# Optimization experiments

Hardware: AMD Instinct MI355X
Metric: run time of the kernel (lower is better)

Reference implementation:

```python
import jax, jax.numpy as jnp
import numpy as np

N = 50000        # nodes
E = 1600000      # edges (before self loops)
IN_DIM = 300     # input feature size
HID = 256        # hidden size
HEADS = 8
OC = HID // HEADS  # out channels per head = 32
LAYERS = 4
B = 1024         # number of target pairs
C = 3            # num classes
NEG_SLOPE = 0.2  # PyG GATConv leaky_relu slope


def setup_inputs() -> dict:
    key = jax.random.key(0)
    ks = jax.random.split(key, 12)

    def glorot(k, shape):
        lim = np.sqrt(6.0 / (shape[-2] + shape[-1]))
        return jax.random.uniform(k, shape, jnp.float32, -lim, lim)

    return {
        "x": jax.random.normal(ks[0], (N, IN_DIM), jnp.float32),
        "edge_index": jax.random.randint(ks[1], (2, E), 0, N, jnp.int64 if jax.config.jax_enable_x64 else jnp.int32),
        "target_mask": jax.random.randint(ks[2], (B, 2), 0, N, jnp.int64 if jax.config.jax_enable_x64 else jnp.int32),
        # lin1: [IN_DIM, HID] (stored pre-transposed vs torch)
        "lin1_W": glorot(ks[3], (IN_DIM, HID)),
        "lin1_b": jnp.zeros((HID,), jnp.float32),
        # stacked GATConv params
        "convs_W": glorot(ks[4], (LAYERS, HID, HEADS * OC)),
        "convs_att_dst": glorot(ks[5], (LAYERS, HEADS, OC)),  # att half applied to x_i (target)
        "convs_att_src": glorot(ks[6], (LAYERS, HEADS, OC)),  # att half applied to x_j (source)
        "convs_b": jnp.zeros((LAYERS, HID), jnp.float32),
        # lin3: [2*HID, C]
        "lin3_W": glorot(ks[7], (2 * HID, C)),
        "lin3_b": jnp.zeros((C,), jnp.float32),
    }


def gat_layer(h, src, tgt, W, att_dst, att_src, bias):
    """PyG-style GATConv (concat heads), edge list already includes self loops.
    h: [N, HID]; src/tgt: [E+N]; W: [HID, HEADS*OC]."""
    hw = (h @ W).reshape(N, HEADS, OC)
    # per-node attention scores, gathered per-edge (avoids materializing concat features)
    s_dst = jnp.einsum("nho,ho->nh", hw, att_dst)  # score for target role
    s_src = jnp.einsum("nho,ho->nh", hw, att_src)  # score for source role
    alpha = jax.nn.leaky_relu(s_dst[tgt] + s_src[src], NEG_SLOPE)  # [Etot, HEADS]
    # softmax over edges sharing the same target node (self loops => no empty segments)
    m = jax.ops.segment_max(alpha, tgt, num_segments=N)
    ex = jnp.exp(alpha - m[tgt])
    denom = jax.ops.segment_sum(ex, tgt, num_segments=N)
    a = ex / (denom[tgt] + 1e-16)
    # weighted scatter-aggregate of source features
    out = jax.ops.segment_sum(hw[src] * a[:, :, None], tgt, num_segments=N)  # [N, HEADS, OC]
    return out.reshape(N, HEADS * OC) + bias


def reference(x, edge_index, target_mask, lin1_W, lin1_b, convs_W,
              convs_att_dst, convs_att_src, convs_b, lin3_W, lin3_b):
    # add self loops once (PyG GATConv does this per layer; same edge set every layer)
    loop = jnp.arange(N, dtype=edge_index.dtype)
    src = jnp.concatenate([edge_index[0], loop])
    tgt = jnp.concatenate([edge_index[1], loop])

    h = x @ lin1_W + lin1_b
    for l in range(LAYERS):
        h = jax.nn.elu(gat_layer(h, src, tgt, convs_W[l],
                                 convs_att_dst[l], convs_att_src[l], convs_b[l]))
    # gather the two target nodes per sample and flatten -> [B, 2*HID]
    feats = h[target_mask].reshape(B, 2 * HID)
    logits = feats @ lin3_W + lin3_b
    return logits
```

## Files before the change

kernel.cpp:

```cpp
#include <hip/hip_runtime.h>
#include <math.h>

#define N_NODES 50000
#define N_PAD   50048
#define E_EDGES 1600000
#define ETOT    (E_EDGES + N_NODES)
#define EPAD    (E_EDGES + 8 * N_NODES)
#define IN_DIM  300
#define KP1     320
#define HID     256
#define HEADS   8
#define OC      32
#define LAYERS  4
#define BSAMP   1024
#define NEG_SLOPE 0.2f
#define DEG_CAP 128

#define NB     8
#define NPB    6250
#define BCAP   262144
#define NBLK_P 512

typedef unsigned long long ull;
typedef _Float16 half8 __attribute__((ext_vector_type(8)));
typedef _Float16 half4v __attribute__((ext_vector_type(4)));
typedef float f32x4 __attribute__((ext_vector_type(4)));


__global__ __launch_bounds__(256) void part_count_kernel(const int* __restrict__ tgt,
                                                         int* __restrict__ gcount) {
    __shared__ int cnt[NB];
    if (threadIdx.x < NB) cnt[threadIdx.x] = 0;
    __syncthreads();
    const int chunk = (ETOT + NBLK_P - 1) / NBLK_P;
    int beg = blockIdx.x * chunk;
    int end = min(beg + chunk, ETOT);
    for (int e = beg + threadIdx.x; e < end; e += 256) {
        int t_ = (e < E_EDGES) ? tgt[e] : (e - E_EDGES);
        atomicAdd(&cnt[t_ / NPB], 1);
    }
    __syncthreads();
    if (threadIdx.x < NB) gcount[blockIdx.x * NB + threadIdx.x] = cnt[threadIdx.x];
}

__global__ __launch_bounds__(64) void part_scan_kernel(const int* __restrict__ gcount,
                                                       int* __restrict__ goff,
                                                       int* __restrict__ bcnt) {
    int b = threadIdx.x;
    if (b >= NB) return;
    int running = 0;
    for (int k = 0; k < NBLK_P; k++) {
        goff[k * NB + b] = running;
        running += gcount[k * NB + b];
    }
    bcnt[b] = running;
}

__global__ __launch_bounds__(256) void part_scatter_kernel(const int* __restrict__ src,
                                                           const int* __restrict__ tgt,
                                                           const int* __restrict__ goff,
                                                           ull* __restrict__ bpart) {
    __shared__ int cur[NB];
    if (threadIdx.x < NB) cur[threadIdx.x] = goff[blockIdx.x * NB + threadIdx.x];
    __syncthreads();
    const int chunk = (ETOT + NBLK_P - 1) / NBLK_P;
    int beg = blockIdx.x * chunk;
    int end = min(beg + chunk, ETOT);
    for (int e = beg + threadIdx.x; e < end; e += 256) {
        int s_, t_;
        if (e < E_EDGES) { s_ = src[e]; t_ = tgt[e]; }
        else             { s_ = t_ = e - E_EDGES; }
        int b = t_ / NPB;
        int pos = atomicAdd(&cur[b], 1);
        bpart[(size_t)b * BCAP + pos] = ((ull)(unsigned)t_ << 32) | (unsigned)s_;
    }
}

__global__ __launch_bounds__(256) void count_edges_kernel(const ull* __restrict__ bpart,
                                                          const int* __restrict__ bcnt,
                                                          int* counts) {
    int b = blockIdx.x & (NB - 1);
    int ib = blockIdx.x >> 3;
    int nblk = gridDim.x >> 3;
    int nb = bcnt[b];
    const ull* bp = bpart + (size_t)b * BCAP;
    for (int i = ib * 256 + threadIdx.x; i < nb; i += nblk * 256)
        atomicAdd(&counts[(int)(bp[i] >> 32)], 1);
}

__global__ __launch_bounds__(256) void scan_kernel(const int* __restrict__ counts,
                                                   int* __restrict__ row_ptr,
                                                   int* __restrict__ cursor) {
    __shared__ int sums[256];
    const int CHUNK = (N_NODES + 255) / 256;
    int t = threadIdx.x;
    int beg = t * CHUNK;
    int fin = min(beg + CHUNK, N_NODES);
    int s = 0;
    for (int i = beg; i < fin; i++) s += (counts[i] + 7) & ~7;
    sums[t] = s;
    __syncthreads();
    for (int off = 1; off < 256; off <<= 1) {
        int a = sums[t];
        int u = (t >= off) ? sums[t - off] : 0;
        __syncthreads();
        sums[t] = a + u;
        __syncthreads();
    }
    int running = sums[t] - s;
    for (int i = beg; i < fin; i++) {
        row_ptr[i] = running;
        cursor[i]  = running;
        running += (counts[i] + 7) & ~7;
    }
    if (t == 255) row_ptr[N_NODES] = sums[255];
}

__global__ __launch_bounds__(256) void fill_edges_kernel(const ull* __restrict__ bpart,
                                                         const int* __restrict__ bcnt,
                                                         int* cursor, int* __restrict__ col) {
    int b = blockIdx.x & (NB - 1);
    int ib = blockIdx.x >> 3;
    int nblk = gridDim.x >> 3;
    int nb = bcnt[b];
    const ull* bp = bpart + (size_t)b * BCAP;
    for (int i = ib * 256 + threadIdx.x; i < nb; i += nblk * 256) {
        ull pk = bp[i];
        int t_ = (int)(pk >> 32);
        int s_ = (int)pk;
        int pos = atomicAdd(&cursor[t_], 1);
        col[pos] = s_;
    }
}

__global__ __launch_bounds__(256) void pad_edges_kernel(const int* __restrict__ cursor,
                                                        const int* __restrict__ row_ptr,
                                                        int* __restrict__ col) {
    int i = blockIdx.x * 256 + threadIdx.x;
    if (i >= N_NODES) return;
    int e = cursor[i];
    int pe = row_ptr[i + 1];
    for (; e < pe; e++) col[e] = i;
}


__global__ __launch_bounds__(256) void cast_x_kernel(const float* __restrict__ x, _Float16* __restrict__ xh) {
    long i = (long)blockIdx.x * 256 + threadIdx.x;
    if (i >= (long)N_NODES * KP1) return;
    int r = (int)(i / KP1), c = (int)(i % KP1);
    float v = (c < IN_DIM) ? x[(size_t)r * IN_DIM + c] : 0.f;
    xh[i] = (_Float16)v;
}

__global__ __launch_bounds__(256) void cast_w1_kernel(const float* __restrict__ W, _Float16* __restrict__ Wt) {
    int i = blockIdx.x * 256 + threadIdx.x;
    if (i >= HID * KP1) return;
    int n = i / KP1, k = i % KP1;
    float v = (k < IN_DIM) ? W[(size_t)k * HID + n] : 0.f;
    Wt[i] = (_Float16)v;
}

__global__ __launch_bounds__(256) void cast_wc_kernel(const float* __restrict__ W, _Float16* __restrict__ Wt) {
    int i = blockIdx.x * 256 + threadIdx.x;
    if (i >= LAYERS * HID * HID) return;
    int l = i / (HID * HID);
    int r = i % (HID * HID);
    int n = r / HID, k = r % HID;
    Wt[i] = (_Float16)W[(size_t)l * HID * HID + (size_t)k * HID + n];
}

__global__ __launch_bounds__(256) void gemm_mfma_kernel(const _Float16* __restrict__ A,
                                                        const _Float16* __restrict__ Wt,
                                                        const float* __restrict__ bias,
                                                        _Float16* __restrict__ C,
                                                        int M, int Kp, int addbias) {
    __shared__ _Float16 As[128][32];
    __shared__ _Float16 Bs[128][32];
    const int tid = threadIdx.x;
    const int m0 = blockIdx.x * 128;
    const int n0 = blockIdx.y * 128;
    const int w = tid >> 6, lane = tid & 63;
    const int wm = (w & 1) * 64, wn = (w >> 1) * 64;
    const int quad = lane >> 4, m16 = lane & 15;

    f32x4 acc[4][4];
    #pragma unroll
    for (int i = 0; i < 4; i++)
        #pragma unroll
        for (int j = 0; j < 4; j++)
            acc[i][j] = (f32x4){0.f, 0.f, 0.f, 0.f};

    for (int k0 = 0; k0 < Kp; k0 += 32) {
        #pragma unroll
        for (int i = 0; i < 2; i++) {
            int seg = tid + i * 256;
            int row = seg >> 2, off = seg & 3;
            uint4 v = *(const uint4*)&A[(size_t)(m0 + row) * Kp + k0 + off * 8];
            *(uint4*)&As[row][off * 8] = v;
            uint4 u = *(const uint4*)&Wt[(size_t)(n0 + row) * Kp + k0 + off * 8];
            *(uint4*)&Bs[row][off * 8] = u;
        }
        __syncthreads();

        half8 af[4], bf[4];
        #pragma unroll
        for (int i = 0; i < 4; i++) {
            af[i] = *(const half8*)&As[wm + i * 16 + m16][quad * 8];
            bf[i] = *(const half8*)&Bs[wn + i * 16 + m16][quad * 8];
        }
        #pragma unroll
        for (int mi = 0; mi < 4; mi++)
            #pragma unroll
            for (int ni = 0; ni < 4; ni++)
                acc[mi][ni] = __builtin_amdgcn_mfma_f32_16x16x32_f16(af[mi], bf[ni], acc[mi][ni], 0, 0, 0);
        __syncthreads();
    }

    #pragma unroll
    for (int mi = 0; mi < 4; mi++) {
        #pragma unroll
        for (int r = 0; r < 4; r++) {
            int row = m0 + wm + mi * 16 + quad * 4 + r;
            if (row < M) {
                #pragma unroll
                for (int ni = 0; ni < 4; ni++) {
                    int colg = n0 + wn + ni * 16 + m16;
                    float v = acc[mi][ni][r];
                    if (addbias) v += bias[colg];
                    C[(size_t)row * HID + colg] = (_Float16)v;
                }
            }
        }
    }
}

__global__ __launch_bounds__(256) void score_kernel(const _Float16* __restrict__ hw,
                                                    const float* __restrict__ att_dst,
                                                    const float* __restrict__ att_src,
                                                    float* __restrict__ s_dst,
                                                    float* __restrict__ s_src) {
    int wv = threadIdx.x >> 6, lane = threadIdx.x & 63;
    int nd = lane >> 3, hd = lane & 7;
    float4 ad[8], as4[8];
    const float4* A4d = (const float4*)att_dst;
    const float4* A4s = (const float4*)att_src;
    #pragma unroll
    for (int j = 0; j < 8; j++) { ad[j] = A4d[hd * 8 + j]; as4[j] = A4s[hd * 8 + j]; }
    const half8* hw8 = (const half8*)hw;
    int nwaves = gridDim.x * 4;
    for (int g = blockIdx.x * 4 + wv; g < N_NODES / 8; g += nwaves) {
        int node = g * 8 + nd;
        float sd = 0.f, ss = 0.f;
        #pragma unroll
        for (int k = 0; k < 4; k++) {
            half8 v = hw8[(size_t)node * 32 + hd * 4 + k];
            #pragma unroll
            for (int i = 0; i < 8; i++) {
                float f = (float)v[i];
                int q = k * 8 + i;
                sd += f * ((const float*)&ad[q >> 2])[q & 3];
                ss += f * ((const float*)&as4[q >> 2])[q & 3];
            }
        }
        s_dst[(size_t)g * 64 + lane] = sd;
        s_src[(size_t)g * 64 + lane] = ss;
    }
}

__global__ __launch_bounds__(256) void agg_kernel(const int* __restrict__ row_ptr,
                                                  const int* __restrict__ deg_arr,
                                                  const int* __restrict__ col,
                                                  const float* __restrict__ s_dst,
                                                  const float* __restrict__ s_src,
                                                  const _Float16* __restrict__ hw,
                                                  const float* __restrict__ bias,
                                                  _Float16* __restrict__ h_out) {
    __shared__ float exL[4][DEG_CAP * 8];
    __shared__ int  snL[4][DEG_CAP];

    int wv   = threadIdx.x >> 6;
    int lane = threadIdx.x & 63;
    int t = blockIdx.x * 4 + wv;
    if (t >= N_NODES) return;

    int start = row_ptr[t];
    int pdeg  = row_ptr[t + 1] - start;
    int deg   = deg_arr[t];

    int eh  = lane & 7;
    int ech = lane >> 3;
    float sd = s_dst[(size_t)t * HEADS + eh];

    if (pdeg <= DEG_CAP) {
        int ngrp = pdeg >> 3;
        float dsum = 0.f;
        for (int g = 0; g < ngrp; g++) {
            int slot = g * 8 + ech;
            int sn = col[start + slot];
            float a = sd + s_src[(size_t)sn * HEADS + eh];
            a = (a > 0.f) ? a : NEG_SLOPE * a;
            float exv = (slot < deg) ? __expf(a) : 0.f;
            exL[wv][slot * 8 + eh] = exv;
            if (eh == 0) snL[wv][slot] = sn;
            dsum += exv;
        }
        dsum += __shfl_xor(dsum, 8);
        dsum += __shfl_xor(dsum, 16);
        dsum += __shfl_xor(dsum, 32);

        int p  = lane >> 5;
        int c  = lane & 31;
        int hh = c >> 2;
        float inv = 1.f / (__shfl(dsum, hh) + 1e-16f);

        const half8* hw8 = (const half8*)hw;
        float acc[8] = {0.f, 0.f, 0.f, 0.f, 0.f, 0.f, 0.f, 0.f};

        for (int g = 0; g < ngrp; g++) {
            int base = g * 8;
            int   sns[4];
            half8 v[4];
            float ex[4];
            #pragma unroll
            for (int j = 0; j < 4; j++) sns[j] = snL[wv][base + 2 * j + p];
            #pragma unroll
            for (int j = 0; j < 4; j++) v[j] = hw8[(size_t)sns[j] * 32 + c];
            #pragma unroll
            for (int j = 0; j < 4; j++) ex[j] = exL[wv][(base + 2 * j + p) * 8 + hh];
            #pragma unroll
            for (int j = 0; j < 4; j++)
                #pragma unroll
                for (int i = 0; i < 8; i++)
                    acc[i] += ex[j] * (float)v[j][i];
        }

        #pragma unroll
        for (int i = 0; i < 8; i++) acc[i] += __shfl_xor(acc[i], 32);

        if (p == 0) {
            half8 ov;
            #pragma unroll
            for (int i = 0; i < 8; i++) {
                float o = acc[i] * inv + bias[c * 8 + i];
                o = (o > 0.f) ? o : (__expf(o) - 1.f);
                ov[i] = (_Float16)o;
            }
            ((half8*)h_out)[(size_t)t * 32 + c] = ov;
        }
    } else {
        int end = start + deg;
        float mx = -1e30f;
        for (int base = start; base < end; base += 8) {
            int e = base + ech;
            if (e < end) {
                int sn = col[e];
                float a = sd + s_src[(size_t)sn * HEADS + eh];
                a = (a > 0.f) ? a : NEG_SLOPE * a;
                mx = fmaxf(mx, a);
            }
        }
        mx = fmaxf(mx, __shfl_xor(mx, 8));
        mx = fmaxf(mx, __shfl_xor(mx, 16));
        mx = fmaxf(mx, __shfl_xor(mx, 32));

        float4 acc = {0.f, 0.f, 0.f, 0.f};
        float dsum = 0.f;
        const half4v* hw4 = (const half4v*)hw;
        int chead = lane >> 3;
        for (int base = start; base < end; base += 8) {
            int e = base + ech;
            float exv = 0.f;
            int sn = 0;
            if (e < end) {
                sn = col[e];
                float a = sd + s_src[(size_t)sn * HEADS + eh];
                a = (a > 0.f) ? a : NEG_SLOPE * a;
                exv = __expf(a - mx);
                dsum += exv;
            }
            int cnt = min(8, end - base);
            for (int j = 0; j < cnt; j++) {
                float exj = __shfl(exv, j * 8 + chead);
                int  snj  = __shfl(sn,  j * 8);
                half4v v = hw4[(size_t)snj * 64 + lane];
                acc.x += exj * (float)v[0];
                acc.y += exj * (float)v[1];
                acc.z += exj * (float)v[2];
                acc.w += exj * (float)v[3];
            }
        }
        dsum += __shfl_xor(dsum, 8);
        dsum += __shfl_xor(dsum, 16);
        dsum += __shfl_xor(dsum, 32);
        float den = __shfl(dsum, chead) + 1e-16f;
        float inv = 1.f / den;
        int cb = lane * 4;
        float o[4] = {acc.x * inv + bias[cb + 0], acc.y * inv + bias[cb + 1],
                      acc.z * inv + bias[cb + 2], acc.w * inv + bias[cb + 3]};
        #pragma unroll
        for (int i = 0; i < 4; i++) o[i] = (o[i] > 0.f) ? o[i] : (__expf(o[i]) - 1.f);
        half4v ov;
        ov[0] = (_Float16)o[0]; ov[1] = (_Float16)o[1];
        ov[2] = (_Float16)o[2]; ov[3] = (_Float16)o[3];
        ((half4v*)h_out)[(size_t)t * 64 + lane] = ov;
    }
}

__global__ __launch_bounds__(256) void head_kernel(const _Float16* __restrict__ h,
                                                   const int* __restrict__ target_mask,
                                                   const float* __restrict__ W,
                                                   const float* __restrict__ b,
                                                   float* __restrict__ out) {
    int s = blockIdx.x;
    int t = threadIdx.x;
    int n0 = target_mask[s * 2 + 0];
    int n1 = target_mask[s * 2 + 1];
    float f0 = (float)h[(size_t)n0 * HID + t];
    float f1 = (float)h[(size_t)n1 * HID + t];
    float a0 = f0 * W[t * 3 + 0] + f1 * W[(t + 256) * 3 + 0];
    float a1 = f0 * W[t * 3 + 1] + f1 * W[(t + 256) * 3 + 1];
    float a2 = f0 * W[t * 3 + 2] + f1 * W[(t + 256) * 3 + 2];
    #pragma unroll
    for (int off = 32; off >= 1; off >>= 1) {
        a0 += __shfl_xor(a0, off);
        a1 += __shfl_xor(a1, off);
        a2 += __shfl_xor(a2, off);
    }
    __shared__ float red[4][3];
    int wv = t >> 6, ln = t & 63;
    if (ln == 0) { red[wv][0] = a0; red[wv][1] = a1; red[wv][2] = a2; }
    __syncthreads();
    if (t < 3) {
        out[s * 3 + t] = red[0][t] + red[1][t] + red[2][t] + red[3][t] + b[t];
    }
}


extern "C" void kernel_launch(void* const* d_in, const int* in_sizes, int n_in,
                              void* d_out, int out_size, void* d_ws, size_t ws_size,
                              hipStream_t stream) {
    const float* x        = (const float*)d_in[0];
    const int*   eidx     = (const int*)  d_in[1];
    const int*   tmask    = (const int*)  d_in[2];
    const float* lin1_W   = (const float*)d_in[3];
    const float* lin1_b   = (const float*)d_in[4];
    const float* convs_W  = (const float*)d_in[5];
    const float* att_dst  = (const float*)d_in[6];
    const float* att_src  = (const float*)d_in[7];
    const float* convs_b  = (const float*)d_in[8];
    const float* lin3_W   = (const float*)d_in[9];
    const float* lin3_b   = (const float*)d_in[10];
    float* out = (float*)d_out;

    char* ws = (char*)d_ws;
    size_t off = 0;
    auto alloc = [&](size_t bytes) -> void* {
        void* p = ws + off;
        off = (off + bytes + 255) & ~(size_t)255;
        return p;
    };
    _Float16* xh   = (_Float16*)alloc((size_t)N_PAD * KP1 * 2);
    _Float16* h    = (_Float16*)alloc((size_t)N_PAD * HID * 2);
    _Float16* hw   = (_Float16*)alloc((size_t)N_NODES * HID * 2);
    _Float16* w1t  = (_Float16*)alloc((size_t)HID * KP1 * 2);
    _Float16* wct  = (_Float16*)alloc((size_t)LAYERS * HID * HID * 2);
    float* sdst    = (float*)alloc((size_t)N_NODES * HEADS * 4);
    float* ssrc    = (float*)alloc((size_t)N_NODES * HEADS * 4);
    int*   counts  = (int*)  alloc((size_t)N_NODES * 4);
    int*   rowptr  = (int*)  alloc((size_t)(N_NODES + 1) * 4);
    int*   cursor  = (int*)  alloc((size_t)N_NODES * 4);
    int*   col     = (int*)  alloc((size_t)EPAD * 4);
    ull*   bpart   = (ull*)  alloc((size_t)NB * BCAP * 8);
    int*   bcnt    = (int*)  alloc((size_t)NB * 4);
    int*   gcount  = (int*)  alloc((size_t)NBLK_P * NB * 4);
    int*   goff    = (int*)  alloc((size_t)NBLK_P * NB * 4);

    const int* src = eidx;
    const int* tgt = eidx + E_EDGES;

    hipMemsetAsync(counts, 0, (size_t)N_NODES * 4, stream);
    part_count_kernel<<<NBLK_P, 256, 0, stream>>>(tgt, gcount);
    part_scan_kernel<<<1, 64, 0, stream>>>(gcount, goff, bcnt);
    part_scatter_kernel<<<NBLK_P, 256, 0, stream>>>(src, tgt, goff, bpart);
    count_edges_kernel<<<256, 256, 0, stream>>>(bpart, bcnt, counts);
    scan_kernel<<<1, 256, 0, stream>>>(counts, rowptr, cursor);
    fill_edges_kernel<<<256, 256, 0, stream>>>(bpart, bcnt, cursor, col);
    pad_edges_kernel<<<(N_NODES + 255) / 256, 256, 0, stream>>>(cursor, rowptr, col);

    cast_x_kernel<<<((long)N_NODES * KP1 + 255) / 256, 256, 0, stream>>>(x, xh);
    cast_w1_kernel<<<(HID * KP1 + 255) / 256, 256, 0, stream>>>(lin1_W, w1t);
    cast_wc_kernel<<<(LAYERS * HID * HID + 255) / 256, 256, 0, stream>>>(convs_W, wct);

    gemm_mfma_kernel<<<dim3((N_NODES + 127) / 128, HID / 128), 256, 0, stream>>>(
        xh, w1t, lin1_b, h, N_NODES, KP1, 1);

    for (int l = 0; l < LAYERS; l++) {
        gemm_mfma_kernel<<<dim3((N_NODES + 127) / 128, HID / 128), 256, 0, stream>>>(
            h, wct + (size_t)l * HID * HID, nullptr, hw, N_NODES, HID, 0);
        score_kernel<<<256, 256, 0, stream>>>(
            hw, att_dst + (size_t)l * HEADS * OC, att_src + (size_t)l * HEADS * OC, sdst, ssrc);
        agg_kernel<<<(N_NODES + 3) / 4, 256, 0, stream>>>(
            rowptr, counts, col, sdst, ssrc, hw, convs_b + (size_t)l * HID, h);
    }

    head_kernel<<<BSAMP, 256, 0, stream>>>(h, tmask, lin3_W, lin3_b, out);
}
```

Measured before the change: 1.076 ms.

## Parallelize row-pointer scan, use direct global-to-LDS loads in GEMM, unroll aggregation

Replaces the single-block serial scan over node degrees with a three-kernel multi-block scan: per-block scan, scan of block sums, then an add-back. The GEMM tile loads now use global_load_lds, copying straight into shared memory without passing through registers. The aggregation loop processes 8 neighbour rows per iteration instead of 4, so more gathers are in flight at once. The unrolled loop adds register pressure, the scan adds two launches, and the LDS-direct load depends on the address layout matching the per-wave 1 KB placement.

```diff
diff --git a/kernel.cpp b/kernel.cpp
--- a/kernel.cpp
+++ b/kernel.cpp
@@ -20,11 +20,16 @@
 #define NPB    6250
 #define BCAP   262144
 #define NBLK_P 512
+#define NBLK_S 196
 
 typedef unsigned long long ull;
 typedef _Float16 half8 __attribute__((ext_vector_type(8)));
 typedef _Float16 half4v __attribute__((ext_vector_type(4)));
 typedef float f32x4 __attribute__((ext_vector_type(4)));
+
+#define GLDS16(g, l) __builtin_amdgcn_global_load_lds( \
+    (const __attribute__((address_space(1))) void*)(g), \
+    (__attribute__((address_space(3))) void*)(l), 16, 0, 0)
 
 
 __global__ __launch_bounds__(256) void part_count_kernel(const int* __restrict__ tgt,
@@ -88,17 +93,14 @@
         atomicAdd(&counts[(int)(bp[i] >> 32)], 1);
 }
 
-__global__ __launch_bounds__(256) void scan_kernel(const int* __restrict__ counts,
-                                                   int* __restrict__ row_ptr,
-                                                   int* __restrict__ cursor) {
+__global__ __launch_bounds__(256) void scan1_kernel(const int* __restrict__ counts,
+                                                    int* __restrict__ row_ptr,
+                                                    int* __restrict__ bsum) {
     __shared__ int sums[256];
-    const int CHUNK = (N_NODES + 255) / 256;
     int t = threadIdx.x;
-    int beg = t * CHUNK;
-    int fin = min(beg + CHUNK, N_NODES);
-    int s = 0;
-    for (int i = beg; i < fin; i++) s += (counts[i] + 7) & ~7;
-    sums[t] = s;
+    int i = blockIdx.x * 256 + t;
+    int c = (i < N_NODES) ? ((counts[i] + 7) & ~7) : 0;
+    sums[t] = c;
     __syncthreads();
     for (int off = 1; off < 256; off <<= 1) {
         int a = sums[t];
@@ -107,13 +109,37 @@
         sums[t] = a + u;
         __syncthreads();
     }
-    int running = sums[t] - s;
-    for (int i = beg; i < fin; i++) {
-        row_ptr[i] = running;
-        cursor[i]  = running;
-        running += (counts[i] + 7) & ~7;
-    }
+    if (i < N_NODES) row_ptr[i] = sums[t] - c;
+    if (t == 255) bsum[blockIdx.x] = sums[255];
+}
+
+__global__ __launch_bounds__(256) void scan2_kernel(const int* __restrict__ bsum,
+                                                    int* __restrict__ boff,
+                                                    int* __restrict__ row_ptr) {
+    __shared__ int sums[256];
+    int t = threadIdx.x;
+    int b = (t < NBLK_S) ? bsum[t] : 0;
+    sums[t] = b;
+    __syncthreads();
+    for (int off = 1; off < 256; off <<= 1) {
+        int a = sums[t];
+        int u = (t >= off) ? sums[t - off] : 0;
+        __syncthreads();
+        sums[t] = a + u;
+        __syncthreads();
+    }
+    if (t < NBLK_S) boff[t] = sums[t] - b;
     if (t == 255) row_ptr[N_NODES] = sums[255];
+}
+
+__global__ __launch_bounds__(256) void scan3_kernel(int* __restrict__ row_ptr,
+                                                    const int* __restrict__ boff,
+                                                    int* __restrict__ cursor) {
+    int i = blockIdx.x * 256 + threadIdx.x;
+    if (i >= N_NODES) return;
+    int v = row_ptr[i] + boff[blockIdx.x];
+    row_ptr[i] = v;
+    cursor[i]  = v;
 }
 
 __global__ __launch_bounds__(256) void fill_edges_kernel(const ull* __restrict__ bpart,
@@ -190,15 +216,16 @@
         for (int j = 0; j < 4; j++)
             acc[i][j] = (f32x4){0.f, 0.f, 0.f, 0.f};
 
+    char* lA = (char*)&As[0][0] + w * 1024;
+    char* lB = (char*)&Bs[0][0] + w * 1024;
+
     for (int k0 = 0; k0 < Kp; k0 += 32) {
         #pragma unroll
         for (int i = 0; i < 2; i++) {
             int seg = tid + i * 256;
             int row = seg >> 2, off = seg & 3;
-            uint4 v = *(const uint4*)&A[(size_t)(m0 + row) * Kp + k0 + off * 8];
-            *(uint4*)&As[row][off * 8] = v;
-            uint4 u = *(const uint4*)&Wt[(size_t)(n0 + row) * Kp + k0 + off * 8];
-            *(uint4*)&Bs[row][off * 8] = u;
+            GLDS16(&A[(size_t)(m0 + row) * Kp + k0 + off * 8], lA + i * 4096);
+            GLDS16(&Wt[(size_t)(n0 + row) * Kp + k0 + off * 8], lB + i * 4096);
         }
         __syncthreads();
 
@@ -316,7 +343,25 @@
         const half8* hw8 = (const half8*)hw;
         float acc[8] = {0.f, 0.f, 0.f, 0.f, 0.f, 0.f, 0.f, 0.f};
 
-        for (int g = 0; g < ngrp; g++) {
+        int g = 0;
+        for (; g + 2 <= ngrp; g += 2) {
+            int base = g * 8;
+            int   sns[8];
+            half8 v[8];
+            float ex[8];
+            #pragma unroll
+            for (int j = 0; j < 8; j++) sns[j] = snL[wv][base + 2 * j + p];
+            #pragma unroll
+            for (int j = 0; j < 8; j++) v[j] = hw8[(size_t)sns[j] * 32 + c];
+            #pragma unroll
+            for (int j = 0; j < 8; j++) ex[j] = exL[wv][(base + 2 * j + p) * 8 + hh];
+            #pragma unroll
+            for (int j = 0; j < 8; j++)
+                #pragma unroll
+                for (int i = 0; i < 8; i++)
+                    acc[i] += ex[j] * (float)v[j][i];
+        }
+        if (g < ngrp) {
             int base = g * 8;
             int   sns[4];
             half8 v[4];
@@ -474,6 +519,8 @@
     int*   bcnt    = (int*)  alloc((size_t)NB * 4);
     int*   gcount  = (int*)  alloc((size_t)NBLK_P * NB * 4);
     int*   goff    = (int*)  alloc((size_t)NBLK_P * NB * 4);
+    int*   bsum    = (int*)  alloc((size_t)NBLK_S * 4);
+    int*   boff    = (int*)  alloc((size_t)NBLK_S * 4);
 
     const int* src = eidx;
     const int* tgt = eidx + E_EDGES;
@@ -483,7 +530,9 @@
     part_scan_kernel<<<1, 64, 0, stream>>>(gcount, goff, bcnt);
     part_scatter_kernel<<<NBLK_P, 256, 0, stream>>>(src, tgt, goff, bpart);
     count_edges_kernel<<<256, 256, 0, stream>>>(bpart, bcnt, counts);
-    scan_kernel<<<1, 256, 0, stream>>>(counts, rowptr, cursor);
+    scan1_kernel<<<NBLK_S, 256, 0, stream>>>(counts, rowptr, bsum);
+    scan2_kernel<<<1, 256, 0, stream>>>(bsum, boff, rowptr);
+    scan3_kernel<<<NBLK_S, 256, 0, stream>>>(rowptr, boff, cursor);
     fill_edges_kernel<<<256, 256, 0, stream>>>(bpart, bcnt, cursor, col);
     pad_edges_kernel<<<(N_NODES + 255) / 256, 256, 0, stream>>>(cursor, rowptr, col);
 
```

Result: faster. 975.7 us (-9.4%).
